# Kernel tuning notes

Measured on AMD Instinct MI355X. Metric: run time of the kernel, lower is better.

Reference implementation:

```python
import jax, jax.numpy as jnp
import numpy as np

B, S, D, H = 4, 2048, 1024, 16
HD = D // H


def setup_inputs() -> dict:
    key = jax.random.key(0)
    ks = jax.random.split(key, 11)
    s = 1.0 / np.sqrt(D)
    return {
        "query": jax.random.normal(ks[0], (B, S, D), jnp.float32),
        "key": jax.random.normal(ks[1], (B, S, D), jnp.float32),
        "value": jax.random.normal(ks[2], (B, S, D), jnp.float32),
        "Wq": jax.random.normal(ks[3], (D, D), jnp.float32) * s,
        "bq": jax.random.normal(ks[4], (D,), jnp.float32) * s,
        "Wk": jax.random.normal(ks[5], (D, D), jnp.float32) * s,
        "bk": jax.random.normal(ks[6], (D,), jnp.float32) * s,
        "Wv": jax.random.normal(ks[7], (D, D), jnp.float32) * s,
        "bv": jax.random.normal(ks[8], (D,), jnp.float32) * s,
        "Wo": jax.random.normal(ks[9], (D, D), jnp.float32) * s,
        "bo": jax.random.normal(ks[10], (D,), jnp.float32) * s,
    }


def reference(query, key, value, Wq, bq, Wk, bk, Wv, bv, Wo, bo):
    b = query.shape[0]
    # projections (torch Linear: x @ W.T + b)
    q = (query @ Wq.T + bq).reshape(b, -1, H, HD).transpose(0, 2, 1, 3)  # [B,H,S,hd]
    k = (key @ Wk.T + bk).reshape(b, -1, H, HD).transpose(0, 2, 1, 3)
    v = (value @ Wv.T + bv).reshape(b, -1, H, HD).transpose(0, 2, 1, 3)
    scores = jnp.einsum('bhqd,bhkd->bhqk', q, k) / jnp.sqrt(jnp.float32(HD))
    attn = jax.nn.softmax(scores, axis=-1)  # dropout = identity (eval)
    out = jnp.einsum('bhqk,bhkd->bhqd', attn, v)
    out = out.transpose(0, 2, 1, 3).reshape(b, -1, D)
    return out @ Wo.T + bo
```

## Files before the change

kernel.cpp:

```cpp
#include <hip/hip_runtime.h>
#include <stdint.h>

typedef __attribute__((ext_vector_type(8))) short  s16x8;
typedef __attribute__((ext_vector_type(4))) float  f32x4;
typedef __attribute__((ext_vector_type(4))) unsigned short u16x4;

__device__ __forceinline__ unsigned short f2bf(float f) {
  union { float f; uint32_t u; } x; x.f = f;
  uint32_t u = x.u;
  return (unsigned short)((u + 0x7fffu + ((u >> 16) & 1u)) >> 16);
}

__device__ __forceinline__ float fexp2(float x) {
  float r; asm("v_exp_f32 %0, %1" : "=v"(r) : "v"(x)); return r;
}
__device__ __forceinline__ uint32_t cvtpk_bf16(float lo, float hi) {
  uint32_t r; asm("v_cvt_pk_bf16_f32 %0, %1, %2" : "=v"(r) : "v"(lo), "v"(hi)); return r;
}

__device__ __forceinline__ void gload_lds16(const void* g, void* l) {
  __builtin_amdgcn_global_load_lds(
      (const __attribute__((address_space(1))) void*)g,
      (__attribute__((address_space(3))) void*)l, 16, 0, 0);
}

struct CvtJobs {
  const float* src[7];
  unsigned short* dst[7];
  int n4[7];
};
__global__ __launch_bounds__(256) void cvt_all(CvtJobs jobs) {
  const int j = blockIdx.y;
  const float* __restrict__ src = jobs.src[j];
  unsigned short* __restrict__ dst = jobs.dst[j];
  const int n4 = jobs.n4[j];
  const int stride = gridDim.x * blockDim.x;
  for (int i = blockIdx.x * blockDim.x + threadIdx.x; i < n4; i += stride) {
    f32x4 v = *(const f32x4*)(src + (size_t)i * 4);
    u16x4 o = { f2bf(v[0]), f2bf(v[1]), f2bf(v[2]), f2bf(v[3]) };
    *(u16x4*)(dst + (size_t)i * 4) = o;
  }
}

struct GemmJob {
  const unsigned short* A;
  const unsigned short* Bmat;
  const float* bias;
  unsigned short* C;
  int M, N, Nb;
  int bias_row;
  float scale;
};

__device__ __forceinline__ void gemm_core4(const unsigned short* __restrict__ A,
                                           const unsigned short* __restrict__ Bw,
                                           int m0, int n0, int K, char* L,
                                           f32x4 (&acc)[4][4]) {
  const int tid = threadIdx.x;
  const int l = tid & 63;
  const int lr = l & 15, lc = l >> 4;
  const int w = tid >> 6;
  const int wr = w >> 1, wc = w & 1;

  const int srow = tid >> 2;
  const int sc = (tid & 3) ^ ((srow >> 1) & 3);
  const unsigned short* sA1 = A + (size_t)(m0 + srow) * K + sc * 8;
  const unsigned short* sA2 = A + (size_t)(m0 + srow + 64) * K + sc * 8;
  const unsigned short* sB1 = Bw + (size_t)(n0 + srow) * K + sc * 8;
  const unsigned short* sB2 = Bw + (size_t)(n0 + srow + 64) * K + sc * 8;
  char* d1 = L + (size_t)tid * 16;
  char* d2 = d1 + 4096;
  char* d3 = d1 + 8192;
  char* d4 = d1 + 12288;

#define GSTAGE(BUF, KS) { gload_lds16(sA1 + (KS), d1 + (BUF) * 16384); \
                          gload_lds16(sA2 + (KS), d2 + (BUF) * 16384); \
                          gload_lds16(sB1 + (KS), d3 + (BUF) * 16384); \
                          gload_lds16(sB2 + (KS), d4 + (BUF) * 16384); }

  const int s16 = (lc ^ ((lr >> 1) & 3)) * 16;
  int offA[4], offB[4];
#pragma unroll
  for (int i = 0; i < 4; ++i) offA[i] = (wr * 64 + i * 16 + lr) * 64 + s16;
#pragma unroll
  for (int j = 0; j < 4; ++j) offB[j] = 8192 + (wc * 64 + j * 16 + lr) * 64 + s16;

  const int nk = K >> 5;
  GSTAGE(0, 0);
  asm volatile("s_waitcnt vmcnt(0)" ::: "memory");
  __builtin_amdgcn_s_barrier();
  int cur = 0;
  for (int t = 0; t < nk; ++t) {
    if (t + 1 < nk) GSTAGE(cur ^ 1, (t + 1) * 32);
    const char* Lb = L + cur * 16384;
    s16x8 af[4], bfr[4];
#pragma unroll
    for (int i = 0; i < 4; ++i) af[i] = *(const s16x8*)(Lb + offA[i]);
#pragma unroll
    for (int j = 0; j < 4; ++j) bfr[j] = *(const s16x8*)(Lb + offB[j]);
    __builtin_amdgcn_s_setprio(1);
#pragma unroll
    for (int i = 0; i < 4; ++i)
#pragma unroll
      for (int j = 0; j < 4; ++j)
        acc[i][j] = __builtin_amdgcn_mfma_f32_16x16x32_bf16(af[i], bfr[j], acc[i][j], 0, 0, 0);
    __builtin_amdgcn_s_setprio(0);
    asm volatile("s_waitcnt vmcnt(0)" ::: "memory");
    __builtin_amdgcn_s_barrier();
    cur ^= 1;
  }
#undef GSTAGE
}

__global__ __launch_bounds__(256) void gemm_qkv(GemmJob j0, GemmJob j1, GemmJob j2) {
  __shared__ __align__(16) char L[32768];
  const int f = blockIdx.x;
  const int wid = (f & 7) * 192 + (f >> 3);
  const int job = wid >> 9;
  const int i = wid & 511;
  const GemmJob jb = (job == 0) ? j0 : (job == 1) ? j1 : j2;
  const int m0 = (i / jb.Nb) * 128, n0 = (i % jb.Nb) * 128;
  f32x4 acc[4][4];
#pragma unroll
  for (int i2 = 0; i2 < 4; ++i2)
#pragma unroll
    for (int j2 = 0; j2 < 4; ++j2) acc[i2][j2] = (f32x4){0.f, 0.f, 0.f, 0.f};
  gemm_core4(jb.A, jb.Bmat, m0, n0, 1024, L, acc);
  const int tid = threadIdx.x;
  const int l = tid & 63, w = tid >> 6;
  const int lr = l & 15, lc = l >> 4;
  const int wr = w >> 1, wc = w & 1;
#pragma unroll
  for (int i2 = 0; i2 < 4; ++i2) {
    const int row0 = m0 + wr * 64 + i2 * 16 + lc * 4;
    f32x4 brow;
    if (jb.bias_row) brow = *(const f32x4*)&jb.bias[row0];
#pragma unroll
    for (int j2 = 0; j2 < 4; ++j2) {
      const int col = n0 + wc * 64 + j2 * 16 + lr;
      float bcol = jb.bias_row ? 0.f : jb.bias[col];
#pragma unroll
      for (int r = 0; r < 4; ++r) {
        float v = (acc[i2][j2][r] + (jb.bias_row ? brow[r] : bcol)) * jb.scale;
        jb.C[(size_t)(row0 + r) * jb.N + col] = f2bf(v);
      }
    }
  }
}

__global__ __launch_bounds__(256) void gemm_out(const unsigned short* __restrict__ A,
                                                const unsigned short* __restrict__ Bw,
                                                const float* __restrict__ bias,
                                                float* __restrict__ Cout,
                                                int M, int N, int K) {
  __shared__ __align__(16) char L[32768];
  const int f = blockIdx.x;
  const int wid = (f & 7) * 64 + (f >> 3);
  const int m0 = (wid >> 3) * 128, n0 = (wid & 7) * 128;
  f32x4 acc[4][4];
#pragma unroll
  for (int i = 0; i < 4; ++i)
#pragma unroll
    for (int j = 0; j < 4; ++j) acc[i][j] = (f32x4){0.f, 0.f, 0.f, 0.f};
  gemm_core4(A, Bw, m0, n0, K, L, acc);
  const int tid = threadIdx.x;
  const int l = tid & 63, w = tid >> 6;
  const int lr = l & 15, lc = l >> 4;
  const int wr = w >> 1, wc = w & 1;
#pragma unroll
  for (int i = 0; i < 4; ++i) {
    const int row0 = m0 + wr * 64 + i * 16 + lc * 4;
#pragma unroll
    for (int j = 0; j < 4; ++j) {
      const int col = n0 + wc * 64 + j * 16 + lr;
      float bcol = bias[col];
#pragma unroll
      for (int r = 0; r < 4; ++r)
        Cout[(size_t)(row0 + r) * N + col] = acc[i][j][r] + bcol;
    }
  }
}

__global__ __launch_bounds__(512) void attn_fwd(const unsigned short* __restrict__ qb,
                                                const unsigned short* __restrict__ kb,
                                                const unsigned short* __restrict__ vtb,
                                                unsigned short* __restrict__ ob) {
  __shared__ __align__(16) unsigned short L[3 * 8192];
  const int tid = threadIdx.x;
  const int l = tid & 63, w = tid >> 6;
  const int lr = l & 15, lc = l >> 4;
  const int i0 = blockIdx.x;
  const int wid = (i0 & 7) * 128 + (i0 >> 3);
  const int qx = wid & 15;
  const int h = (wid >> 4) & 15;
  const int b = wid >> 8;
  const int q0 = qx * 128;
  const size_t qkbase = ((size_t)b * 2048) * 1024 + (size_t)h * 64;
  const size_t vtbase = (size_t)(h * 64) * 8192 + (size_t)b * 2048;

  s16x8 aq0, aq1;
  {
    const unsigned short* qp = qb + qkbase + (size_t)(q0 + w * 16 + lr) * 1024 + lc * 8;
    aq0 = *(const s16x8*)qp;
    aq1 = *(const s16x8*)(qp + 32);
  }

  union { u16x4 h4[2]; s16x8 v; } onesu;
#pragma unroll
  for (int i = 0; i < 2; ++i) onesu.h4[i] = (u16x4){0x3F80, 0x3F80, 0x3F80, 0x3F80};
  const s16x8 bones = onesu.v;

  f32x4 oacc[4];
  f32x4 oextra = (f32x4){0.f, 0.f, 0.f, 0.f};
#pragma unroll
  for (int nd = 0; nd < 4; ++nd) oacc[nd] = (f32x4){0.f, 0.f, 0.f, 0.f};

  const int role = w >> 2, wk = w & 3;
  const int rl = l >> 3;
  const int cs = (l & 7) ^ rl;
  const int rA = wk * 16 + rl, rB = rA + 8;
#define RHO(rr) (8 * (((rr) >> 2) & 3) + 4 * (((rr) >> 4) & 1) + ((rr) & 3) + 32 * ((rr) >> 5))
  const unsigned short* sA;
  const unsigned short* sB;
  size_t tstep;
  if (role == 0) {
    sA = kb + qkbase + (size_t)RHO(rA) * 1024 + cs * 8;
    sB = kb + qkbase + (size_t)RHO(rB) * 1024 + cs * 8;
    tstep = (size_t)64 * 1024;
  } else {
    sA = vtb + vtbase + (size_t)rA * 8192 + cs * 8;
    sB = vtb + vtbase + (size_t)rB * 8192 + cs * 8;
    tstep = 64;
  }
#undef RHO
  char* dstL = (char*)L + role * 8192 + wk * 2048 + l * 16;

#define STAGE(BUF, T) {                                              \
    gload_lds16(sA + (size_t)(T) * tstep, dstL + (BUF) * 16384);     \
    gload_lds16(sB + (size_t)(T) * tstep, dstL + (BUF) * 16384 + 1024); }

  int off0[4];
#pragma unroll
  for (int ni = 0; ni < 4; ++ni)
    off0[ni] = (ni * 16 + lr) * 128 + ((lc ^ (lr & 7)) * 16);

  STAGE(0, 0);
  STAGE(1, 1);

  int cur = 0;
  for (int t = 0; t < 32; ++t) {
    if (t < 31) asm volatile("s_waitcnt vmcnt(2)" ::: "memory");
    else        asm volatile("s_waitcnt vmcnt(0)" ::: "memory");
    __builtin_amdgcn_s_barrier();
    if (t < 30) {
      int nb = cur + 2; if (nb >= 3) nb -= 3;
      STAGE(nb, t + 2);
    }
    const char* Lb = (const char*)L + cur * 16384;

    f32x4 sf[4];
    __builtin_amdgcn_s_setprio(1);
#pragma unroll
    for (int ni = 0; ni < 4; ++ni) {
      s16x8 k0 = *(const s16x8*)(Lb + off0[ni]);
      s16x8 k1 = *(const s16x8*)(Lb + (off0[ni] ^ 64));
      f32x4 z = (f32x4){0.f, 0.f, 0.f, 0.f};
      z = __builtin_amdgcn_mfma_f32_16x16x32_bf16(k0, aq0, z, 0, 0, 0);
      z = __builtin_amdgcn_mfma_f32_16x16x32_bf16(k1, aq1, z, 0, 0, 0);
      sf[ni] = z;
    }
    __builtin_amdgcn_s_setprio(0);

    union { uint32_t u[4]; s16x8 v; } pa0u, pa1u;
#pragma unroll
    for (int ni = 0; ni < 4; ++ni) {
      float p0 = fexp2(sf[ni][0]);
      float p1 = fexp2(sf[ni][1]);
      float p2 = fexp2(sf[ni][2]);
      float p3 = fexp2(sf[ni][3]);
      uint32_t w0 = cvtpk_bf16(p0, p1);
      uint32_t w1 = cvtpk_bf16(p2, p3);
      if (ni < 2) { pa0u.u[ni * 2] = w0; pa0u.u[ni * 2 + 1] = w1; }
      else        { pa1u.u[(ni - 2) * 2] = w0; pa1u.u[(ni - 2) * 2 + 1] = w1; }
    }

    __builtin_amdgcn_s_setprio(1);
#pragma unroll
    for (int nd = 0; nd < 4; ++nd) {
      s16x8 v0 = *(const s16x8*)(Lb + 8192 + off0[nd]);
      s16x8 v1 = *(const s16x8*)(Lb + 8192 + (off0[nd] ^ 64));
      oacc[nd] = __builtin_amdgcn_mfma_f32_16x16x32_bf16(pa0u.v, v0, oacc[nd], 0, 0, 0);
      oacc[nd] = __builtin_amdgcn_mfma_f32_16x16x32_bf16(pa1u.v, v1, oacc[nd], 0, 0, 0);
    }
    oextra = __builtin_amdgcn_mfma_f32_16x16x32_bf16(pa0u.v, bones, oextra, 0, 0, 0);
    oextra = __builtin_amdgcn_mfma_f32_16x16x32_bf16(pa1u.v, bones, oextra, 0, 0, 0);
    __builtin_amdgcn_s_setprio(0);

    ++cur; if (cur == 3) cur = 0;
  }

  float linv[4];
#pragma unroll
  for (int r = 0; r < 4; ++r) linv[r] = 1.f / oextra[r];
#pragma unroll
  for (int nd = 0; nd < 4; ++nd)
#pragma unroll
    for (int r = 0; r < 4; ++r) {
      int qrow = q0 + w * 16 + lc * 4 + r;
      ob[qkbase + (size_t)qrow * 1024 + nd * 16 + lr] = f2bf(oacc[nd][r] * linv[r]);
    }
#undef STAGE
}

extern "C" void kernel_launch(void* const* d_in, const int* in_sizes, int n_in,
                              void* d_out, int out_size, void* d_ws, size_t ws_size,
                              hipStream_t stream) {
  const float* query = (const float*)d_in[0];
  const float* key_  = (const float*)d_in[1];
  const float* value = (const float*)d_in[2];
  const float* Wq = (const float*)d_in[3];
  const float* bq = (const float*)d_in[4];
  const float* Wk = (const float*)d_in[5];
  const float* bk = (const float*)d_in[6];
  const float* Wv = (const float*)d_in[7];
  const float* bv = (const float*)d_in[8];
  const float* Wo = (const float*)d_in[9];
  const float* bo = (const float*)d_in[10];

  const int MS = 4 * 2048;
  const int D = 1024;
  const size_t NX = (size_t)MS * D;
  const size_t NW = (size_t)D * D;

  const size_t need = (6 * NX + 4 * NW) * 2;
  if (ws_size < need) return;

  unsigned short* ws  = (unsigned short*)d_ws;
  unsigned short* xq  = ws;
  unsigned short* xk  = xq + NX;
  unsigned short* xv  = xk + NX;
  unsigned short* qb_ = xv + NX;
  unsigned short* kb_ = qb_ + NX;
  unsigned short* vtb = kb_ + NX;
  unsigned short* wqb = vtb + NX;
  unsigned short* wkb = wqb + NW;
  unsigned short* wvb = wkb + NW;
  unsigned short* wob = wvb + NW;
  unsigned short* attn = xq;

  CvtJobs cj;
  cj.src[0] = query; cj.dst[0] = xq;  cj.n4[0] = (int)(NX / 4);
  cj.src[1] = key_;  cj.dst[1] = xk;  cj.n4[1] = (int)(NX / 4);
  cj.src[2] = value; cj.dst[2] = xv;  cj.n4[2] = (int)(NX / 4);
  cj.src[3] = Wq;    cj.dst[3] = wqb; cj.n4[3] = (int)(NW / 4);
  cj.src[4] = Wk;    cj.dst[4] = wkb; cj.n4[4] = (int)(NW / 4);
  cj.src[5] = Wv;    cj.dst[5] = wvb; cj.n4[5] = (int)(NW / 4);
  cj.src[6] = Wo;    cj.dst[6] = wob; cj.n4[6] = (int)(NW / 4);
  cvt_all<<<dim3(1024, 7), 256, 0, stream>>>(cj);

  const float qscale = 0.18033688f;
  GemmJob jq = { xq,  wqb, bq, qb_, MS, D,  D / 128,  0, qscale };
  GemmJob jk = { xk,  wkb, bk, kb_, MS, D,  D / 128,  0, 1.f };
  GemmJob jv = { wvb, xv,  bv, vtb, D,  MS, MS / 128, 1, 1.f };
  gemm_qkv<<<dim3(1536), 256, 0, stream>>>(jq, jk, jv);

  attn_fwd<<<dim3(1024), 512, 0, stream>>>(qb_, kb_, vtb, attn);

  gemm_out<<<dim3(512), 256, 0, stream>>>(attn, wob, bo, (float*)d_out, MS, D, D);
}
```

Before: 201.8 us.

## Process two 16-row query groups per wave to reuse K/V fragments

Each attention block now covers 256 query rows instead of 128, with every wave handling two 16-row query groups. The K and V fragments read from LDS are loaded once per tile and reused for both groups, which halves LDS reads and global K/V staging per query row, and the grid shrinks to 512 blocks. The cost is more registers per wave (more accumulators and cached fragments), which may lower occupancy, and fewer blocks to spread across the CUs.

```diff
diff --git a/kernel.cpp b/kernel.cpp
--- a/kernel.cpp
+++ b/kernel.cpp
@@ -190,19 +190,20 @@
   const int l = tid & 63, w = tid >> 6;
   const int lr = l & 15, lc = l >> 4;
   const int i0 = blockIdx.x;
-  const int wid = (i0 & 7) * 128 + (i0 >> 3);
-  const int qx = wid & 15;
-  const int h = (wid >> 4) & 15;
-  const int b = wid >> 8;
-  const int q0 = qx * 128;
+  const int wid = (i0 & 7) * 64 + (i0 >> 3);
+  const int qx = wid & 7;
+  const int h = (wid >> 3) & 15;
+  const int b = wid >> 7;
+  const int q0 = qx * 256;
   const size_t qkbase = ((size_t)b * 2048) * 1024 + (size_t)h * 64;
   const size_t vtbase = (size_t)(h * 64) * 8192 + (size_t)b * 2048;
 
-  s16x8 aq0, aq1;
-  {
-    const unsigned short* qp = qb + qkbase + (size_t)(q0 + w * 16 + lr) * 1024 + lc * 8;
-    aq0 = *(const s16x8*)qp;
-    aq1 = *(const s16x8*)(qp + 32);
+  s16x8 aq[2][2];
+#pragma unroll
+  for (int g = 0; g < 2; ++g) {
+    const unsigned short* qp = qb + qkbase + (size_t)(q0 + w * 32 + g * 16 + lr) * 1024 + lc * 8;
+    aq[g][0] = *(const s16x8*)qp;
+    aq[g][1] = *(const s16x8*)(qp + 32);
   }
 
   union { u16x4 h4[2]; s16x8 v; } onesu;
@@ -210,10 +211,14 @@
   for (int i = 0; i < 2; ++i) onesu.h4[i] = (u16x4){0x3F80, 0x3F80, 0x3F80, 0x3F80};
   const s16x8 bones = onesu.v;
 
-  f32x4 oacc[4];
-  f32x4 oextra = (f32x4){0.f, 0.f, 0.f, 0.f};
-#pragma unroll
-  for (int nd = 0; nd < 4; ++nd) oacc[nd] = (f32x4){0.f, 0.f, 0.f, 0.f};
+  f32x4 oacc[2][4];
+  f32x4 oextra[2];
+#pragma unroll
+  for (int g = 0; g < 2; ++g) {
+    oextra[g] = (f32x4){0.f, 0.f, 0.f, 0.f};
+#pragma unroll
+    for (int nd = 0; nd < 4; ++nd) oacc[g][nd] = (f32x4){0.f, 0.f, 0.f, 0.f};
+  }
 
   const int role = w >> 2, wk = w & 3;
   const int rl = l >> 3;
@@ -258,57 +263,73 @@
     }
     const char* Lb = (const char*)L + cur * 16384;
 
-    f32x4 sf[4];
+    s16x8 kf[4][2];
+#pragma unroll
+    for (int ni = 0; ni < 4; ++ni) {
+      kf[ni][0] = *(const s16x8*)(Lb + off0[ni]);
+      kf[ni][1] = *(const s16x8*)(Lb + (off0[ni] ^ 64));
+    }
+    s16x8 vf[4][2];
+#pragma unroll
+    for (int nd = 0; nd < 4; ++nd) {
+      vf[nd][0] = *(const s16x8*)(Lb + 8192 + off0[nd]);
+      vf[nd][1] = *(const s16x8*)(Lb + 8192 + (off0[nd] ^ 64));
+    }
+
+    f32x4 sf[2][4];
     __builtin_amdgcn_s_setprio(1);
 #pragma unroll
-    for (int ni = 0; ni < 4; ++ni) {
-      s16x8 k0 = *(const s16x8*)(Lb + off0[ni]);
-      s16x8 k1 = *(const s16x8*)(Lb + (off0[ni] ^ 64));
-      f32x4 z = (f32x4){0.f, 0.f, 0.f, 0.f};
-      z = __builtin_amdgcn_mfma_f32_16x16x32_bf16(k0, aq0, z, 0, 0, 0);
-      z = __builtin_amdgcn_mfma_f32_16x16x32_bf16(k1, aq1, z, 0, 0, 0);
-      sf[ni] = z;
-    }
+    for (int g = 0; g < 2; ++g)
+#pragma unroll
+      for (int ni = 0; ni < 4; ++ni) {
+        f32x4 z = (f32x4){0.f, 0.f, 0.f, 0.f};
+        z = __builtin_amdgcn_mfma_f32_16x16x32_bf16(kf[ni][0], aq[g][0], z, 0, 0, 0);
+        z = __builtin_amdgcn_mfma_f32_16x16x32_bf16(kf[ni][1], aq[g][1], z, 0, 0, 0);
+        sf[g][ni] = z;
+      }
     __builtin_amdgcn_s_setprio(0);
 
-    union { uint32_t u[4]; s16x8 v; } pa0u, pa1u;
-#pragma unroll
-    for (int ni = 0; ni < 4; ++ni) {
-      float p0 = fexp2(sf[ni][0]);
-      float p1 = fexp2(sf[ni][1]);
-      float p2 = fexp2(sf[ni][2]);
-      float p3 = fexp2(sf[ni][3]);
-      uint32_t w0 = cvtpk_bf16(p0, p1);
-      uint32_t w1 = cvtpk_bf16(p2, p3);
-      if (ni < 2) { pa0u.u[ni * 2] = w0; pa0u.u[ni * 2 + 1] = w1; }
-      else        { pa1u.u[(ni - 2) * 2] = w0; pa1u.u[(ni - 2) * 2 + 1] = w1; }
-    }
-
-    __builtin_amdgcn_s_setprio(1);
-#pragma unroll
-    for (int nd = 0; nd < 4; ++nd) {
-      s16x8 v0 = *(const s16x8*)(Lb + 8192 + off0[nd]);
-      s16x8 v1 = *(const s16x8*)(Lb + 8192 + (off0[nd] ^ 64));
-      oacc[nd] = __builtin_amdgcn_mfma_f32_16x16x32_bf16(pa0u.v, v0, oacc[nd], 0, 0, 0);
-      oacc[nd] = __builtin_amdgcn_mfma_f32_16x16x32_bf16(pa1u.v, v1, oacc[nd], 0, 0, 0);
-    }
-    oextra = __builtin_amdgcn_mfma_f32_16x16x32_bf16(pa0u.v, bones, oextra, 0, 0, 0);
-    oextra = __builtin_amdgcn_mfma_f32_16x16x32_bf16(pa1u.v, bones, oextra, 0, 0, 0);
-    __builtin_amdgcn_s_setprio(0);
+#pragma unroll
+    for (int g = 0; g < 2; ++g) {
+      union { uint32_t u[4]; s16x8 v; } pa0u, pa1u;
+#pragma unroll
+      for (int ni = 0; ni < 4; ++ni) {
+        float p0 = fexp2(sf[g][ni][0]);
+        float p1 = fexp2(sf[g][ni][1]);
+        float p2 = fexp2(sf[g][ni][2]);
+        float p3 = fexp2(sf[g][ni][3]);
+        uint32_t w0 = cvtpk_bf16(p0, p1);
+        uint32_t w1 = cvtpk_bf16(p2, p3);
+        if (ni < 2) { pa0u.u[ni * 2] = w0; pa0u.u[ni * 2 + 1] = w1; }
+        else        { pa1u.u[(ni - 2) * 2] = w0; pa1u.u[(ni - 2) * 2 + 1] = w1; }
+      }
+      __builtin_amdgcn_s_setprio(1);
+#pragma unroll
+      for (int nd = 0; nd < 4; ++nd) {
+        oacc[g][nd] = __builtin_amdgcn_mfma_f32_16x16x32_bf16(pa0u.v, vf[nd][0], oacc[g][nd], 0, 0, 0);
+        oacc[g][nd] = __builtin_amdgcn_mfma_f32_16x16x32_bf16(pa1u.v, vf[nd][1], oacc[g][nd], 0, 0, 0);
+      }
+      oextra[g] = __builtin_amdgcn_mfma_f32_16x16x32_bf16(pa0u.v, bones, oextra[g], 0, 0, 0);
+      oextra[g] = __builtin_amdgcn_mfma_f32_16x16x32_bf16(pa1u.v, bones, oextra[g], 0, 0, 0);
+      __builtin_amdgcn_s_setprio(0);
+    }
 
     ++cur; if (cur == 3) cur = 0;
   }
 
-  float linv[4];
-#pragma unroll
-  for (int r = 0; r < 4; ++r) linv[r] = 1.f / oextra[r];
-#pragma unroll
-  for (int nd = 0; nd < 4; ++nd)
-#pragma unroll
-    for (int r = 0; r < 4; ++r) {
-      int qrow = q0 + w * 16 + lc * 4 + r;
-      ob[qkbase + (size_t)qrow * 1024 + nd * 16 + lr] = f2bf(oacc[nd][r] * linv[r]);
-    }
+#pragma unroll
+  for (int g = 0; g < 2; ++g) {
+    float linv[4];
+#pragma unroll
+    for (int r = 0; r < 4; ++r) linv[r] = 1.f / oextra[g][r];
+#pragma unroll
+    for (int nd = 0; nd < 4; ++nd)
+#pragma unroll
+      for (int r = 0; r < 4; ++r) {
+        int qrow = q0 + w * 32 + g * 16 + lc * 4 + r;
+        ob[qkbase + (size_t)qrow * 1024 + nd * 16 + lr] = f2bf(oacc[g][nd][r] * linv[r]);
+      }
+  }
 #undef STAGE
 }
 
@@ -364,7 +385,7 @@
   GemmJob jv = { wvb, xv,  bv, vtb, D,  MS, MS / 128, 1, 1.f };
   gemm_qkv<<<dim3(1536), 256, 0, stream>>>(jq, jk, jv);
 
-  attn_fwd<<<dim3(1024), 512, 0, stream>>>(qb_, kb_, vtb, attn);
+  attn_fwd<<<dim3(512), 512, 0, stream>>>(qb_, kb_, vtb, attn);
 
   gemm_out<<<dim3(512), 256, 0, stream>>>(attn, wob, bo, (float*)d_out, MS, D, D);
 }
```

Result: no change. 201.3 us (-0.2%).
